# Kernel tuning notes

Measured on AMD Instinct MI355X. Metric: run time of the kernel, lower is better.

## Reference

```python
import jax, jax.numpy as jnp
import numpy as np


def setup_inputs() -> dict:
    key = jax.random.key(0)
    k1, k2 = jax.random.split(key)
    E, D1, D2 = 512, 4096, 16
    # Center row scaled up, error rows scaled down so lb/ub straddle 0 for a
    # realistic mix of dead / stable-positive / crossing neurons.
    center = jax.random.normal(k1, (1, D1, D2), dtype=jnp.float32) * 3.0
    errs = jax.random.normal(k2, (E - 1, D1, D2), dtype=jnp.float32) * 0.01
    x = jnp.concatenate([center, errs], axis=0)
    return {"x": x}


def reference(x):
    size = x.shape
    E = size[0]
    N = int(np.prod(size[1:]))
    xf = x.reshape(E, N)  # [error_terms, neurons]

    # zonotope bounds
    sum_abs = jnp.sum(jnp.abs(xf[1:]), axis=0)  # [N]
    lb = xf[0] - sum_abs
    ub = xf[0] + sum_abs

    crossing = (lb <= 0) & (ub >= 0)  # neurons needing relaxation
    dead = ub <= 0                    # neurons fully zeroed

    # Faithful to source bug: alpha = ub/ub - lb == 1 - lb (missing parens),
    # valid whenever ub != 0 on crossing neurons (a.s. with float data).
    alpha = jnp.where(crossing, 1.0 - lb, 1.0)  # [N]

    center = jnp.where(crossing, alpha * xf[0] - alpha * lb * 0.5, xf[0])
    rest = jnp.where(crossing[None, :], alpha[None, :] * xf[1:], xf[1:])
    out = jnp.concatenate([center[None, :], rest], axis=0)  # [E, N]

    # zero out columns with ub <= 0 (applied after the crossing update,
    # matching the source's statement order)
    out = jnp.where(dead[None, :], 0.0, out)

    # Source's `if new_error_terms.size():` is always truthy -> same shape out.
    return out.reshape(size)
```

## Files before the change

### kernel.cpp

```cpp
#include <hip/hip_runtime.h>


#define EROWS 512
#define W4 8
#define BLK 1024
#define RSTRIDE (BLK / W4)
#define RPT (EROWS / RSTRIDE)
#define NWAVES (BLK / 64)

__global__ __launch_bounds__(BLK) void ar_fused(const float* __restrict__ x,
                                                float* __restrict__ out, int n4) {
    __shared__ float4 slab[EROWS * W4];
    __shared__ float4 part[NWAVES][W4];
    __shared__ float4 scale4[W4];

    int t = threadIdx.x;
    int cseg  = t & (W4 - 1);
    int rbase = t >> 3;
    int col4 = blockIdx.x * W4 + cseg;

    const float4* xv = (const float4*)x;
    float4* ov = (float4*)out;

    float4 acc = {0.f, 0.f, 0.f, 0.f};
    #pragma unroll
    for (int k = 0; k < RPT; ++k) {
        int row = rbase + k * RSTRIDE;
        float4 v = xv[(size_t)row * n4 + col4];
        slab[row * W4 + cseg] = v;
        if (row != 0) {
            acc.x += fabsf(v.x); acc.y += fabsf(v.y);
            acc.z += fabsf(v.z); acc.w += fabsf(v.w);
        }
    }
    #pragma unroll
    for (int d = W4; d < 64; d <<= 1) {
        acc.x += __shfl_xor(acc.x, d);
        acc.y += __shfl_xor(acc.y, d);
        acc.z += __shfl_xor(acc.z, d);
        acc.w += __shfl_xor(acc.w, d);
    }
    if ((t & 63) < W4) part[t >> 6][cseg] = acc;
    __syncthreads();

    if (t < W4) {
        float4 s = {0.f, 0.f, 0.f, 0.f};
        #pragma unroll
        for (int w = 0; w < NWAVES; ++w) {
            float4 p = part[w][t];
            s.x += p.x; s.y += p.y; s.z += p.z; s.w += p.w;
        }
        float4 x0v = slab[t];
        float x0[4] = {x0v.x, x0v.y, x0v.z, x0v.w};
        float sm[4] = {s.x, s.y, s.z, s.w};
        float sc[4], o0[4];
        #pragma unroll
        for (int j = 0; j < 4; ++j) {
            float lb = x0[j] - sm[j];
            float ub = x0[j] + sm[j];
            bool crossing = (lb <= 0.f) && (ub >= 0.f);
            bool dead = (ub <= 0.f);
            float alpha = crossing ? (1.f - lb) : 1.f;
            float scl = dead ? 0.f : (crossing ? alpha : 1.f);
            float addv = (crossing && !dead) ? (-alpha * lb * 0.5f) : 0.f;
            sc[j] = scl;
            o0[j] = scl * x0[j] + addv;
        }
        float4 scv = {sc[0], sc[1], sc[2], sc[3]};
        float4 o0v = {o0[0], o0[1], o0[2], o0[3]};
        scale4[t] = scv;
        ov[col4] = o0v;
    }
    __syncthreads();

    float4 s = scale4[cseg];
    #pragma unroll
    for (int k = 0; k < RPT; ++k) {
        int row = rbase + k * RSTRIDE;
        if (row == 0) continue;
        float4 v = slab[row * W4 + cseg];
        float4 o;
        o.x = v.x * s.x; o.y = v.y * s.y;
        o.z = v.z * s.z; o.w = v.w * s.w;
        ov[(size_t)row * n4 + col4] = o;
    }
}

extern "C" void kernel_launch(void* const* d_in, const int* in_sizes, int n_in,
                              void* d_out, int out_size, void* d_ws, size_t ws_size,
                              hipStream_t stream) {
    const float* x = (const float*)d_in[0];
    float* out = (float*)d_out;
    int total = in_sizes[0];
    int N = total / EROWS;
    int n4 = N >> 2;
    int nblocks = n4 / W4;

    ar_fused<<<nblocks, BLK, 0, stream>>>(x, out, n4);
}
```

Measured before the change: 46.60 us.

## Double-buffer column groups with direct global-to-LDS async loads

Each block now covers 8 groups of 4 float4 columns instead of one 8-column slab. It loads the next group straight into a second LDS buffer with global_load_lds while the current group is reduced, scaled and stored. The aim is to overlap load latency with the reduction and the stores, and to skip the register round-trip into shared memory. In exchange, each row access is a narrower 64-byte segment, there are 4x fewer blocks, and the manual waitcnt and barrier sequencing is fragile.

```diff
diff --git a/kernel.cpp b/kernel.cpp
--- a/kernel.cpp
+++ b/kernel.cpp
@@ -2,87 +2,126 @@
 
 
 #define EROWS 512
-#define W4 8
+#define CSEG 4
+#define NG 8
 #define BLK 1024
-#define RSTRIDE (BLK / W4)
-#define RPT (EROWS / RSTRIDE)
 #define NWAVES (BLK / 64)
 
-__global__ __launch_bounds__(BLK) void ar_fused(const float* __restrict__ x,
-                                                float* __restrict__ out, int n4) {
-    __shared__ float4 slab[EROWS * W4];
-    __shared__ float4 part[NWAVES][W4];
-    __shared__ float4 scale4[W4];
+__global__ __launch_bounds__(BLK) void ar_pipe(const float* __restrict__ x,
+                                               float* __restrict__ out, int n4) {
+    __shared__ float4 buf[2][EROWS * CSEG];
+    __shared__ float4 part[NWAVES][CSEG];
+    __shared__ float4 scale4[CSEG];
 
-    int t = threadIdx.x;
-    int cseg  = t & (W4 - 1);
-    int rbase = t >> 3;
-    int col4 = blockIdx.x * W4 + cseg;
-
+    const int t    = threadIdx.x;
+    const int cseg = t & (CSEG - 1);
+    const int rh   = t >> 2;
+    const int w    = t >> 6;
+    const int lane = t & 63;
     const float4* xv = (const float4*)x;
     float4* ov = (float4*)out;
 
-    float4 acc = {0.f, 0.f, 0.f, 0.f};
-    #pragma unroll
-    for (int k = 0; k < RPT; ++k) {
-        int row = rbase + k * RSTRIDE;
-        float4 v = xv[(size_t)row * n4 + col4];
-        slab[row * W4 + cseg] = v;
-        if (row != 0) {
-            acc.x += fabsf(v.x); acc.y += fabsf(v.y);
-            acc.z += fabsf(v.z); acc.w += fabsf(v.w);
+    const int col4_base = blockIdx.x * (NG * CSEG);
+
+    auto stage = [&](int g, int b) {
+        const int col4_0 = col4_base + g * CSEG;
+        #pragma unroll
+        for (int i = 0; i < 2; ++i) {
+            const int rowbase = w * 32 + i * 16;
+            const int row = rowbase + (lane >> 2);
+            const float4* gsrc = xv + (size_t)row * n4 + col4_0 + (lane & 3);
+            float4* ldst = &buf[b][rowbase * CSEG];
+            __builtin_amdgcn_global_load_lds(
+                (const __attribute__((address_space(1))) void*)gsrc,
+                (__attribute__((address_space(3))) void*)ldst,
+                16, 0, 0);
         }
-    }
-    #pragma unroll
-    for (int d = W4; d < 64; d <<= 1) {
-        acc.x += __shfl_xor(acc.x, d);
-        acc.y += __shfl_xor(acc.y, d);
-        acc.z += __shfl_xor(acc.z, d);
-        acc.w += __shfl_xor(acc.w, d);
-    }
-    if ((t & 63) < W4) part[t >> 6][cseg] = acc;
-    __syncthreads();
+    };
 
-    if (t < W4) {
-        float4 s = {0.f, 0.f, 0.f, 0.f};
+    stage(0, 0);
+    asm volatile("s_waitcnt vmcnt(0)" ::: "memory");
+    __builtin_amdgcn_s_barrier();
+    asm volatile("" ::: "memory");
+
+    #pragma unroll 1
+    for (int g = 0; g < NG; ++g) {
+        const int b = g & 1;
+        const int col4_0 = col4_base + g * CSEG;
+
+        if (g + 1 < NG) stage(g + 1, b ^ 1);
+
+        float4 v0 = buf[b][t];
+        float4 v1 = buf[b][t + 1024];
+
+        float4 acc;
+        acc.x = fabsf(v1.x); acc.y = fabsf(v1.y);
+        acc.z = fabsf(v1.z); acc.w = fabsf(v1.w);
+        if (t >= CSEG) {
+            acc.x += fabsf(v0.x); acc.y += fabsf(v0.y);
+            acc.z += fabsf(v0.z); acc.w += fabsf(v0.w);
+        }
         #pragma unroll
-        for (int w = 0; w < NWAVES; ++w) {
-            float4 p = part[w][t];
-            s.x += p.x; s.y += p.y; s.z += p.z; s.w += p.w;
+        for (int d = CSEG; d < 64; d <<= 1) {
+            acc.x += __shfl_xor(acc.x, d);
+            acc.y += __shfl_xor(acc.y, d);
+            acc.z += __shfl_xor(acc.z, d);
+            acc.w += __shfl_xor(acc.w, d);
         }
-        float4 x0v = slab[t];
-        float x0[4] = {x0v.x, x0v.y, x0v.z, x0v.w};
-        float sm[4] = {s.x, s.y, s.z, s.w};
-        float sc[4], o0[4];
-        #pragma unroll
-        for (int j = 0; j < 4; ++j) {
-            float lb = x0[j] - sm[j];
-            float ub = x0[j] + sm[j];
-            bool crossing = (lb <= 0.f) && (ub >= 0.f);
-            bool dead = (ub <= 0.f);
-            float alpha = crossing ? (1.f - lb) : 1.f;
-            float scl = dead ? 0.f : (crossing ? alpha : 1.f);
-            float addv = (crossing && !dead) ? (-alpha * lb * 0.5f) : 0.f;
-            sc[j] = scl;
-            o0[j] = scl * x0[j] + addv;
+        if (lane < CSEG) part[w][lane] = acc;
+
+        asm volatile("s_waitcnt lgkmcnt(0)" ::: "memory");
+        __builtin_amdgcn_s_barrier();
+        asm volatile("" ::: "memory");
+
+        if (t < CSEG) {
+            float sm[4] = {0.f, 0.f, 0.f, 0.f};
+            #pragma unroll
+            for (int wv = 0; wv < NWAVES; ++wv) {
+                float4 p = part[wv][t];
+                sm[0] += p.x; sm[1] += p.y; sm[2] += p.z; sm[3] += p.w;
+            }
+            float x0[4] = {v0.x, v0.y, v0.z, v0.w};
+            float sc[4], o0[4];
+            #pragma unroll
+            for (int j = 0; j < 4; ++j) {
+                float lb = x0[j] - sm[j];
+                float ub = x0[j] + sm[j];
+                bool crossing = (lb <= 0.f) && (ub >= 0.f);
+                bool dead = (ub <= 0.f);
+                float alpha = crossing ? (1.f - lb) : 1.f;
+                float scl = dead ? 0.f : (crossing ? alpha : 1.f);
+                float addv = (crossing && !dead) ? (-alpha * lb * 0.5f) : 0.f;
+                sc[j] = scl;
+                o0[j] = scl * x0[j] + addv;
+            }
+            float4 scv = {sc[0], sc[1], sc[2], sc[3]};
+            float4 o0v = {o0[0], o0[1], o0[2], o0[3]};
+            scale4[t] = scv;
+            ov[col4_0 + t] = o0v;
         }
-        float4 scv = {sc[0], sc[1], sc[2], sc[3]};
-        float4 o0v = {o0[0], o0[1], o0[2], o0[3]};
-        scale4[t] = scv;
-        ov[col4] = o0v;
-    }
-    __syncthreads();
+        asm volatile("s_waitcnt lgkmcnt(0)" ::: "memory");
+        __builtin_amdgcn_s_barrier();
+        asm volatile("" ::: "memory");
 
-    float4 s = scale4[cseg];
-    #pragma unroll
-    for (int k = 0; k < RPT; ++k) {
-        int row = rbase + k * RSTRIDE;
-        if (row == 0) continue;
-        float4 v = slab[row * W4 + cseg];
-        float4 o;
-        o.x = v.x * s.x; o.y = v.y * s.y;
-        o.z = v.z * s.z; o.w = v.w * s.w;
-        ov[(size_t)row * n4 + col4] = o;
+        float4 s = scale4[cseg];
+        if (t >= CSEG) {
+            float4 o;
+            o.x = v0.x * s.x; o.y = v0.y * s.y;
+            o.z = v0.z * s.z; o.w = v0.w * s.w;
+            ov[(size_t)rh * n4 + col4_0 + cseg] = o;
+        }
+        {
+            float4 o;
+            o.x = v1.x * s.x; o.y = v1.y * s.y;
+            o.z = v1.z * s.z; o.w = v1.w * s.w;
+            ov[(size_t)(rh + 256) * n4 + col4_0 + cseg] = o;
+        }
+
+        if (g + 1 < NG) {
+            asm volatile("s_waitcnt vmcnt(2)" ::: "memory");
+        }
+        __builtin_amdgcn_s_barrier();
+        asm volatile("" ::: "memory");
     }
 }
 
@@ -94,7 +133,7 @@
     int total = in_sizes[0];
     int N = total / EROWS;
     int n4 = N >> 2;
-    int nblocks = n4 / W4;
+    int nblocks = n4 / (NG * CSEG);
 
-    ar_fused<<<nblocks, BLK, 0, stream>>>(x, out, n4);
+    ar_pipe<<<nblocks, BLK, 0, stream>>>(x, out, n4);
 }
```

After: 67.79 us. 45.5% more time.
